# Kernel optimization log

Hardware: AMD Instinct MI355X
Metric: run time of the kernel (lower is better)

Reference implementation:

```python
import jax, jax.numpy as jnp
import numpy as np

B, N, M, D_MODEL, D_K, D_V = 8, 2048, 2048, 1024, 1024, 1024
NEG = -1000000000.0


def setup_inputs() -> dict:
    key = jax.random.key(0)
    ks = jax.random.split(key, 10)
    s = 1.0 / np.sqrt(D_MODEL)
    return {
        "querys": jax.random.normal(ks[0], (B, N, D_MODEL), jnp.float32),
        "keys": jax.random.normal(ks[1], (B, M, D_MODEL), jnp.float32),
        "values": jax.random.normal(ks[2], (B, M, D_MODEL), jnp.float32),
        "mask": jax.random.randint(ks[3], (N, M), 0, 2, jnp.int32),
        "Wq": jax.random.normal(ks[4], (D_K, D_MODEL), jnp.float32) * s,
        "bq": jnp.zeros((D_K,), jnp.float32),
        "Wk": jax.random.normal(ks[5], (D_K, D_MODEL), jnp.float32) * s,
        "bk": jnp.zeros((D_K,), jnp.float32),
        "Wv": jax.random.normal(ks[6], (D_V, D_MODEL), jnp.float32) * s,
        "bv": jnp.zeros((D_V,), jnp.float32),
    }


def reference(querys, keys, values, mask, Wq, bq, Wk, bk, Wv, bv):
    # Linear projections (torch Linear: x @ W.T + b)
    q = querys @ Wq.T + bq          # [B, N, Dk]
    k = keys @ Wk.T + bk            # [B, M, Dk]
    v = values @ Wv.T + bv          # [B, M, Dv]
    # Original computes QK^T via broadcast mul+sum; GEMM form is identical math.
    # NOTE: no 1/sqrt(d) scaling, matching the source.
    scores = jnp.einsum('bnd,bmd->bnm', q, k)  # [B, N, M]
    scores = jnp.where(mask[None, :, :] == 0, NEG, scores)
    weights = jax.nn.softmax(scores, axis=2)
    out = jnp.einsum('bnm,bmd->bnd', weights, v)  # [B, N, Dv]
    return out
```

## Files before the change

### kernel.cpp

```cpp
#include <hip/hip_runtime.h>
#include <cstdint>

typedef __bf16 bf16_t;
typedef __bf16 bf16x8 __attribute__((ext_vector_type(8)));
typedef float f32x4 __attribute__((ext_vector_type(4)));

#define AS1 __attribute__((address_space(1)))
#define AS3 __attribute__((address_space(3)))

__device__ __forceinline__ void gload_lds16(const bf16_t* g, bf16_t* l) {
    __builtin_amdgcn_global_load_lds((const AS1 void*)g, (AS3 void*)l, 16, 0, 0);
}
__device__ __forceinline__ f32x4 mfma_bf16(bf16x8 a, bf16x8 b, f32x4 c) {
    return __builtin_amdgcn_mfma_f32_16x16x32_bf16(a, b, c, 0, 0, 0);
}

template <bool SPLIT, int BIAS, int OUTMODE>
__global__ __launch_bounds__(512, 2) void gemm256(
    const bf16_t* __restrict__ Ah, const bf16_t* __restrict__ Al, long long strideA, int lda,
    const bf16_t* __restrict__ Bh, const bf16_t* __restrict__ Bl, long long strideB, int ldb,
    void* __restrict__ C0, void* __restrict__ C1, long long strideC, int ldc,
    const float* __restrict__ bias, int K)
{
    __shared__ bf16_t lds[4 * 16384];

    const int bz = blockIdx.z;
    const int rowBase = blockIdx.y * 256;
    const int colBase = blockIdx.x * 256;
    const bf16_t* AhB = Ah + (long long)bz * strideA;
    const bf16_t* BhB = Bh + (long long)bz * strideB;
    const bf16_t* AlB = SPLIT ? Al + (long long)bz * strideA : nullptr;
    const bf16_t* BlB = SPLIT ? Bl + (long long)bz * strideB : nullptr;

    const int t = threadIdx.x;
    const int lane = t & 63;
    const int w = t >> 6;
    const int wm = w >> 2;
    const int wn = w & 3;

    const int r0 = t >> 2;
    const int sl8 = ((t & 3) ^ ((r0 >> 1) & 3)) * 8;
    const long long aoff0 = (long long)(rowBase + r0) * lda + sl8;
    const long long aoff1 = (long long)(rowBase + r0 + 128) * lda + sl8;
    const long long boff0 = (long long)(colBase + r0) * ldb + sl8;
    const long long boff1 = (long long)(colBase + r0 + 128) * ldb + sl8;

    const int NT = SPLIT ? (K >> 5) * 3 : (K >> 5);

    auto tsrc = [&](int jt, const bf16_t*& sA, const bf16_t*& sB, long long& k0) {
        if (SPLIT) {
            const int chunk = jt / 3;
            const int term = jt - chunk * 3;
            k0 = (long long)chunk * 32;
            sA = (term == 2) ? AlB : AhB;
            sB = (term == 1) ? BlB : BhB;
        } else {
            k0 = (long long)jt * 32;
            sA = AhB; sB = BhB;
        }
    };

    f32x4 acc[8][4] = {};

    for (int jt = 0; jt < 3; ++jt) {
        const bf16_t *sA, *sB; long long k0;
        tsrc(jt, sA, sB, k0);
        bf16_t* db = lds + jt * 16384;
        gload_lds16(sA + aoff0 + k0, db + t * 8);
        gload_lds16(sA + aoff1 + k0, db + 4096 + t * 8);
        gload_lds16(sB + boff0 + k0, db + 8192 + t * 8);
        gload_lds16(sB + boff1 + k0, db + 12288 + t * 8);
    }
    asm volatile("s_waitcnt vmcnt(8)" ::: "memory");
    __builtin_amdgcn_s_barrier();

    const int fr = lane & 15;
    const int kqs = ((lane >> 4) ^ ((lane >> 1) & 3)) * 8;

    for (int j = 0; j < NT; ++j) {
        const bf16_t* bufA = lds + (j & 3) * 16384;
        const bf16_t* bufB = bufA + 8192;
        const int jt = j + 3;
        const bool doStage = jt < NT;
        const bf16_t *sA = nullptr, *sB = nullptr; long long k0 = 0;
        if (doStage) tsrc(jt, sA, sB, k0);
        bf16_t* db = lds + (jt & 3) * 16384;

        bf16x8 a[4], b[4];
#pragma unroll
        for (int mi = 0; mi < 4; mi++)
            a[mi] = *(const bf16x8*)&bufA[(wm * 128 + mi * 16 + fr) * 32 + kqs];
#pragma unroll
        for (int ni = 0; ni < 4; ni++)
            b[ni] = *(const bf16x8*)&bufB[(wn * 64 + ni * 16 + fr) * 32 + kqs];
        if (doStage) {
            gload_lds16(sA + aoff0 + k0, db + t * 8);
            gload_lds16(sA + aoff1 + k0, db + 4096 + t * 8);
        }
        asm volatile("" ::: "memory");
        __builtin_amdgcn_s_barrier();
        __builtin_amdgcn_s_setprio(1);
#pragma unroll
        for (int mi = 0; mi < 4; mi++)
#pragma unroll
            for (int ni = 0; ni < 4; ni++)
                acc[mi][ni] = mfma_bf16(a[mi], b[ni], acc[mi][ni]);
        __builtin_amdgcn_s_setprio(0);
        asm volatile("" ::: "memory");
        __builtin_amdgcn_s_barrier();
#pragma unroll
        for (int mi = 0; mi < 4; mi++)
            a[mi] = *(const bf16x8*)&bufA[(wm * 128 + (mi + 4) * 16 + fr) * 32 + kqs];
        if (doStage) {
            gload_lds16(sB + boff0 + k0, db + 8192 + t * 8);
            gload_lds16(sB + boff1 + k0, db + 12288 + t * 8);
        }
        asm volatile("" ::: "memory");
        __builtin_amdgcn_s_barrier();
        __builtin_amdgcn_s_setprio(1);
#pragma unroll
        for (int mi = 0; mi < 4; mi++)
#pragma unroll
            for (int ni = 0; ni < 4; ni++)
                acc[mi + 4][ni] = mfma_bf16(a[mi], b[ni], acc[mi + 4][ni]);
        __builtin_amdgcn_s_setprio(0);
        if (j + 1 < NT) {
            if (j < NT - 3)       asm volatile("s_waitcnt vmcnt(8)" ::: "memory");
            else if (j == NT - 3) asm volatile("s_waitcnt vmcnt(4)" ::: "memory");
            else                  asm volatile("s_waitcnt vmcnt(0)" ::: "memory");
            __builtin_amdgcn_s_barrier();
        }
    }

    const int fc = lane & 15;
    const int fr4 = (lane >> 4) * 4;
#pragma unroll
    for (int mi = 0; mi < 8; mi++)
#pragma unroll
        for (int ni = 0; ni < 4; ni++)
#pragma unroll
            for (int rg = 0; rg < 4; rg++) {
                const int row = rowBase + wm * 128 + mi * 16 + fr4 + rg;
                const int col = colBase + wn * 64 + ni * 16 + fc;
                float v = acc[mi][ni][rg];
                if (BIAS == 1) v += bias[col];
                else if (BIAS == 2) v += bias[row];
                const long long off = (long long)bz * strideC + (long long)row * ldc + col;
                if (OUTMODE == 0) {
                    ((float*)C0)[off] = v;
                } else if (OUTMODE == 1) {
                    ((bf16_t*)C0)[off] = (bf16_t)v;
                } else {
                    const bf16_t h = (bf16_t)v;
                    ((bf16_t*)C0)[off] = h;
                    ((bf16_t*)C1)[off] = (bf16_t)(v - (float)h);
                }
            }
}

__global__ __launch_bounds__(256) void split_f32(const float* __restrict__ x,
                                                 bf16_t* __restrict__ h,
                                                 bf16_t* __restrict__ l)
{
    const long long i = ((long long)blockIdx.x * 256 + threadIdx.x) * 4;
    const float4 v = *(const float4*)&x[i];
    bf16_t hh[4], ll[4];
    const float vv[4] = {v.x, v.y, v.z, v.w};
#pragma unroll
    for (int j = 0; j < 4; j++) {
        hh[j] = (bf16_t)vv[j];
        ll[j] = (bf16_t)(vv[j] - (float)hh[j]);
    }
    *(short4*)&h[i] = *(short4*)hh;
    *(short4*)&l[i] = *(short4*)ll;
}

__global__ __launch_bounds__(256) void cast_f32(const float* __restrict__ x,
                                                bf16_t* __restrict__ y)
{
    const long long i = ((long long)blockIdx.x * 256 + threadIdx.x) * 4;
    const float4 v = *(const float4*)&x[i];
    bf16_t hh[4] = {(bf16_t)v.x, (bf16_t)v.y, (bf16_t)v.z, (bf16_t)v.w};
    *(short4*)&y[i] = *(short4*)hh;
}

__global__ __launch_bounds__(256) void softmax_rows(const float* __restrict__ S,
                                                    bf16_t* __restrict__ P,
                                                    const int* __restrict__ mask,
                                                    int n0)
{
    __shared__ float red[4];
    const long long r = blockIdx.x;
    const float* row = S + r * 2048;
    const int* mrow = mask + (long long)(n0 + (int)(r & 2047)) * 2048;
    const int t = threadIdx.x;

    float v[8];
#pragma unroll
    for (int i = 0; i < 8; i++) {
        const int j = i * 256 + t;
        v[i] = (mrow[j] != 0) ? row[j] : -1000000000.0f;
    }
    float m = v[0];
#pragma unroll
    for (int i = 1; i < 8; i++) m = fmaxf(m, v[i]);
#pragma unroll
    for (int off = 32; off; off >>= 1) m = fmaxf(m, __shfl_xor(m, off));
    if ((t & 63) == 0) red[t >> 6] = m;
    __syncthreads();
    const float rowmax = fmaxf(fmaxf(red[0], red[1]), fmaxf(red[2], red[3]));
    __syncthreads();

    float sum = 0.0f;
    float e[8];
#pragma unroll
    for (int i = 0; i < 8; i++) { e[i] = __expf(v[i] - rowmax); sum += e[i]; }
#pragma unroll
    for (int off = 32; off; off >>= 1) sum += __shfl_xor(sum, off);
    if ((t & 63) == 0) red[t >> 6] = sum;
    __syncthreads();
    const float inv = 1.0f / (red[0] + red[1] + red[2] + red[3]);

    bf16_t* prow = P + r * 2048;
#pragma unroll
    for (int i = 0; i < 8; i++) prow[i * 256 + t] = (bf16_t)(e[i] * inv);
}

extern "C" void kernel_launch(void* const* d_in, const int* in_sizes, int n_in,
                              void* d_out, int out_size, void* d_ws, size_t ws_size,
                              hipStream_t stream) {
    constexpr int Bb = 8, N = 2048, M = 2048, D = 1024;
    constexpr long long MB = 1LL << 20;

    const float* querys = (const float*)d_in[0];
    const float* keys   = (const float*)d_in[1];
    const float* values = (const float*)d_in[2];
    const int*   mask   = (const int*)d_in[3];
    const float* Wq = (const float*)d_in[4];
    const float* bq = (const float*)d_in[5];
    const float* Wk = (const float*)d_in[6];
    const float* bk = (const float*)d_in[7];
    const float* Wv = (const float*)d_in[8];
    const float* bv = (const float*)d_in[9];
    float* out = (float*)d_out;

    const long long w = (long long)ws_size;
    auto needB = [&](long long cb) { return 10 * MB + cb * 52 * MB; };
    int CB = 0;
    if      (w >= needB(8)) CB = 8;
    else if (w >= needB(4)) CB = 4;
    else if (w >= needB(2)) CB = 2;
    else if (w >= needB(1)) CB = 1;
    const bool batched = (CB != 0);
    int NCH = N;
    if (!batched) {
        CB = 1;
        NCH = (w >= 38 * MB + 512 * 2048 * 6) ? 512 : 256;
    }

    char* ws = (char*)d_ws;
    long long o = 0;
    auto carve = [&](long long bytes) { char* p = ws + o; o += bytes; return p; };
    bf16_t* WqH = (bf16_t*)carve(2 * MB);
    bf16_t* WqL = (bf16_t*)carve(2 * MB);
    bf16_t* WkH = (bf16_t*)carve(2 * MB);
    bf16_t* WkL = (bf16_t*)carve(2 * MB);
    bf16_t* WvB = (bf16_t*)carve(2 * MB);
    bf16_t* XH  = (bf16_t*)carve((long long)CB * 4 * MB);
    bf16_t* XL  = (bf16_t*)carve((long long)CB * 4 * MB);
    bf16_t* QH  = (bf16_t*)carve((long long)CB * 4 * MB);
    bf16_t* QL  = (bf16_t*)carve((long long)CB * 4 * MB);
    bf16_t* KH  = (bf16_t*)carve((long long)CB * 4 * MB);
    bf16_t* KL  = (bf16_t*)carve((long long)CB * 4 * MB);
    bf16_t* VT  = (bf16_t*)carve((long long)CB * 4 * MB);
    float*  S   = (float*)carve(batched ? (long long)CB * N * M * 4 : (long long)NCH * 2048 * 4);
    bf16_t* P   = (bf16_t*)carve(batched ? (long long)CB * N * M * 2 : (long long)NCH * 2048 * 2);

    dim3 blk(256), blkG(512);
    const long long grpElems = (long long)CB * N * D;

    split_f32<<<dim3((D * D) / 1024), blk, 0, stream>>>(Wq, WqH, WqL);
    split_f32<<<dim3((D * D) / 1024), blk, 0, stream>>>(Wk, WkH, WkL);
    cast_f32<<<dim3((D * D) / 1024), blk, 0, stream>>>(Wv, WvB);

    for (int b0 = 0; b0 < Bb; b0 += CB) {
        const long long xoff = (long long)b0 * N * D;
        split_f32<<<dim3(grpElems / 1024), blk, 0, stream>>>(querys + xoff, XH, XL);
        gemm256<true, 1, 2><<<dim3(D / 256, CB * N / 256, 1), blkG, 0, stream>>>(
            XH, XL, 0, D, WqH, WqL, 0, D, QH, QL, 0, D, bq, D);
        split_f32<<<dim3(grpElems / 1024), blk, 0, stream>>>(keys + xoff, XH, XL);
        gemm256<true, 1, 2><<<dim3(D / 256, CB * M / 256, 1), blkG, 0, stream>>>(
            XH, XL, 0, D, WkH, WkL, 0, D, KH, KL, 0, D, bk, D);
        cast_f32<<<dim3(grpElems / 1024), blk, 0, stream>>>(values + xoff, XH);
        gemm256<false, 2, 1><<<dim3(M / 256, D / 256, CB), blkG, 0, stream>>>(
            WvB, nullptr, 0, D, XH, nullptr, (long long)M * D, D,
            VT, nullptr, (long long)D * M, M, bv, D);

        if (batched) {
            gemm256<true, 0, 0><<<dim3(M / 256, N / 256, CB), blkG, 0, stream>>>(
                QH, QL, (long long)N * D, D,
                KH, KL, (long long)M * D, D,
                S, nullptr, (long long)N * M, M, nullptr, D);
            softmax_rows<<<dim3(CB * N), blk, 0, stream>>>(S, P, mask, 0);
            gemm256<false, 0, 0><<<dim3(D / 256, N / 256, CB), blkG, 0, stream>>>(
                P, nullptr, (long long)N * M, M,
                VT, nullptr, (long long)D * M, M,
                out + xoff, nullptr, (long long)N * D, D, nullptr, M);
        } else {
            for (int z = 0; z < CB; z++) {
                for (int n0 = 0; n0 < N; n0 += NCH) {
                    gemm256<true, 0, 0><<<dim3(M / 256, NCH / 256, 1), blkG, 0, stream>>>(
                        QH + ((long long)z * N + n0) * D, QL + ((long long)z * N + n0) * D, 0, D,
                        KH + (long long)z * M * D, KL + (long long)z * M * D, 0, D,
                        S, nullptr, 0, M, nullptr, D);
                    softmax_rows<<<dim3(NCH), blk, 0, stream>>>(S, P, mask, n0);
                    gemm256<false, 0, 0><<<dim3(D / 256, NCH / 256, 1), blkG, 0, stream>>>(
                        P, nullptr, 0, M, VT + (long long)z * D * M, nullptr, 0, M,
                        out + ((long long)(b0 + z) * N + n0) * D, nullptr, 0, D, nullptr, M);
                }
            }
        }
    }
    (void)in_sizes; (void)n_in; (void)out_size;
}
```

Baseline: 1.069 ms.

## Remap block IDs across XCDs and collapse GEMM main loop into single phase

Adds a block-index permutation so consecutive linear blocks are spread across the eight XCDs in contiguous chunks, aiming for better L2 locality of shared A/B tiles. It also restructures the k-loop from two half-phases, each with barriers and interleaved global-to-LDS staging, into one phase that issues all four staging loads up front, then loads all eight A fragments and runs 32 MFMAs. This removes two barriers per iteration but raises register pressure (eight A fragments held at once) and drops the fine-grained interleaving of loads with compute.

```diff
diff --git a/kernel.cpp b/kernel.cpp
--- a/kernel.cpp
+++ b/kernel.cpp
@@ -24,9 +24,20 @@
 {
     __shared__ bf16_t lds[4 * 16384];
 
-    const int bz = blockIdx.z;
-    const int rowBase = blockIdx.y * 256;
-    const int colBase = blockIdx.x * 256;
+    int bx = blockIdx.x, by = blockIdx.y, bz = blockIdx.z;
+    {
+        const int gx = gridDim.x, gy = gridDim.y, gz = gridDim.z;
+        const int n = gx * gy * gz;
+        if ((n & 7) == 0) {
+            int lin = bx + gx * (by + gy * bz);
+            lin = (lin & 7) * (n >> 3) + (lin >> 3);
+            bx = lin % gx; lin /= gx;
+            by = lin % gy; bz = lin / gy;
+        }
+    }
+
+    const int rowBase = by * 256;
+    const int colBase = bx * 256;
     const bf16_t* AhB = Ah + (long long)bz * strideA;
     const bf16_t* BhB = Bh + (long long)bz * strideB;
     const bf16_t* AlB = SPLIT ? Al + (long long)bz * strideA : nullptr;
@@ -80,50 +91,34 @@
     for (int j = 0; j < NT; ++j) {
         const bf16_t* bufA = lds + (j & 3) * 16384;
         const bf16_t* bufB = bufA + 8192;
+
         const int jt = j + 3;
-        const bool doStage = jt < NT;
-        const bf16_t *sA = nullptr, *sB = nullptr; long long k0 = 0;
-        if (doStage) tsrc(jt, sA, sB, k0);
-        bf16_t* db = lds + (jt & 3) * 16384;
-
-        bf16x8 a[4], b[4];
-#pragma unroll
-        for (int mi = 0; mi < 4; mi++)
+        if (jt < NT) {
+            const bf16_t *sA, *sB; long long k0;
+            tsrc(jt, sA, sB, k0);
+            bf16_t* db = lds + (jt & 3) * 16384;
+            gload_lds16(sA + aoff0 + k0, db + t * 8);
+            gload_lds16(sA + aoff1 + k0, db + 4096 + t * 8);
+            gload_lds16(sB + boff0 + k0, db + 8192 + t * 8);
+            gload_lds16(sB + boff1 + k0, db + 12288 + t * 8);
+        }
+
+        bf16x8 a[8], b[4];
+#pragma unroll
+        for (int mi = 0; mi < 8; mi++)
             a[mi] = *(const bf16x8*)&bufA[(wm * 128 + mi * 16 + fr) * 32 + kqs];
 #pragma unroll
         for (int ni = 0; ni < 4; ni++)
             b[ni] = *(const bf16x8*)&bufB[(wn * 64 + ni * 16 + fr) * 32 + kqs];
-        if (doStage) {
-            gload_lds16(sA + aoff0 + k0, db + t * 8);
-            gload_lds16(sA + aoff1 + k0, db + 4096 + t * 8);
-        }
-        asm volatile("" ::: "memory");
-        __builtin_amdgcn_s_barrier();
+
         __builtin_amdgcn_s_setprio(1);
 #pragma unroll
-        for (int mi = 0; mi < 4; mi++)
+        for (int mi = 0; mi < 8; mi++)
 #pragma unroll
             for (int ni = 0; ni < 4; ni++)
                 acc[mi][ni] = mfma_bf16(a[mi], b[ni], acc[mi][ni]);
         __builtin_amdgcn_s_setprio(0);
-        asm volatile("" ::: "memory");
-        __builtin_amdgcn_s_barrier();
-#pragma unroll
-        for (int mi = 0; mi < 4; mi++)
-            a[mi] = *(const bf16x8*)&bufA[(wm * 128 + (mi + 4) * 16 + fr) * 32 + kqs];
-        if (doStage) {
-            gload_lds16(sB + boff0 + k0, db + 8192 + t * 8);
-            gload_lds16(sB + boff1 + k0, db + 12288 + t * 8);
-        }
-        asm volatile("" ::: "memory");
-        __builtin_amdgcn_s_barrier();
-        __builtin_amdgcn_s_setprio(1);
-#pragma unroll
-        for (int mi = 0; mi < 4; mi++)
-#pragma unroll
-            for (int ni = 0; ni < 4; ni++)
-                acc[mi + 4][ni] = mfma_bf16(a[mi], b[ni], acc[mi + 4][ni]);
-        __builtin_amdgcn_s_setprio(0);
+
         if (j + 1 < NT) {
             if (j < NT - 3)       asm volatile("s_waitcnt vmcnt(8)" ::: "memory");
             else if (j == NT - 3) asm volatile("s_waitcnt vmcnt(4)" ::: "memory");
```

Result: faster. 1.005 ms (-6.0%).
